# Kernel tuning notes

Hardware: AMD Instinct MI355X
Metric: run time of the kernel (lower is better)

Reference implementation:

```python
import jax, jax.numpy as jnp
import numpy as np

B, I, D = 4096, 512, 2048
MAX_DIM = 2560
LEAK_RATE = 0.2
SPIKE_THRESHOLD = 0.5


def setup_inputs() -> dict:
    key = jax.random.key(0)
    k1, k2, k3, k4, k5 = jax.random.split(key, 5)
    return {
        "inputs": jax.random.normal(k1, (B, I), dtype=jnp.float32),
        "state": jax.random.normal(k2, (B, MAX_DIM), dtype=jnp.float32),
        "W_in": jax.random.normal(k3, (D, I), dtype=jnp.float32) * 0.05,
        "W_res": jax.random.normal(k4, (D, D), dtype=jnp.float32) * 0.02,
        "W_gate": jax.random.normal(k5, (3 * D, I), dtype=jnp.float32) * 0.05,
    }


def reference(inputs, state, W_in, W_res, W_gate):
    # Slice previous state to the active reservoir dimension D.
    prev_state = state[:, :D]                                   # [B, D]
    input_part = inputs @ W_in.T                                 # [B, D]
    reservoir_part = prev_state @ W_res.T                        # [B, D]
    gate_part = jax.nn.sigmoid(inputs @ W_gate.T)                # [B, 3D]
    i_gate, f_gate, o_gate = jnp.split(gate_part, 3, axis=-1)
    new_state = (1.0 - LEAK_RATE) * (f_gate * prev_state) \
        + LEAK_RATE * jnp.tanh(i_gate * (input_part + reservoir_part))
    new_state = o_gate * new_state
    # Spike thresholding: subtract threshold where state exceeds it.
    new_state = jnp.where(new_state > SPIKE_THRESHOLD,
                          new_state - SPIKE_THRESHOLD, new_state)
    # Zero-pad active reservoir back to max_dynamic_reservoir_dim.
    padded = jnp.pad(new_state, ((0, 0), (0, MAX_DIM - D)))      # [B, MAX_DIM]
    return padded
```

## Files before the change

kernel.cpp:

```cpp
#include <hip/hip_runtime.h>
#include <math.h>


#define IDIM 512
#define DDIM 2048
#define MAXD 2560
#define BDIM 4096
#define LIST_CAP 262144
#define BAND 4e-3f

typedef __attribute__((ext_vector_type(4))) float f32x4;
typedef __attribute__((ext_vector_type(8))) _Float16 f16x8;

__device__ __forceinline__ void gld16(const unsigned short* g, unsigned short* l) {
    __builtin_amdgcn_global_load_lds((const __attribute__((address_space(1))) void*)g,
                                     (__attribute__((address_space(3))) void*)l,
                                     16, 0, 0);
}
__device__ __forceinline__ float sigf(float x) { return 1.0f / (1.0f + __expf(-x)); }

__global__ __launch_bounds__(256) void convert_kernel(
    const float* __restrict__ x, const float* __restrict__ state,
    const float* __restrict__ win, const float* __restrict__ wgate,
    const float* __restrict__ wres,
    unsigned short* __restrict__ X16, unsigned short* __restrict__ S16,
    unsigned short* __restrict__ Wc16, unsigned short* __restrict__ Wr16,
    float* __restrict__ out, unsigned* __restrict__ cnt)
{
    int idx = blockIdx.x * 256 + threadIdx.x;
    if (idx == 0) *cnt = 0u;
    float4 v;
    unsigned short* p;
    long off;
    if (idx < 524288) {
        v = ((const float4*)x)[idx];
        p = X16; off = (long)idx * 4;
    } else if (idx < 2621440) {
        int i = idx - 524288;
        int row = i >> 9, c4 = i & 511;
        v = *(const float4*)(state + (long)row * MAXD + c4 * 4);
        p = S16; off = (long)i * 4;
    } else if (idx < 3670016) {
        int i = idx - 2621440;
        v = (i < 262144) ? ((const float4*)win)[i] : ((const float4*)wgate)[i - 262144];
        p = Wc16; off = (long)i * 4;
    } else if (idx < 4718592) {
        int i = idx - 3670016;
        v = ((const float4*)wres)[i];
        p = Wr16; off = (long)i * 4;
    } else {
        int i = idx - 4718592;
        int row = i >> 7, c4 = i & 127;
        *(float4*)(out + (long)row * MAXD + DDIM + c4 * 4) = make_float4(0.f, 0.f, 0.f, 0.f);
        return;
    }
    _Float16 h0 = (_Float16)v.x, h1 = (_Float16)v.y;
    _Float16 h2 = (_Float16)v.z, h3 = (_Float16)v.w;
    ushort4 hv;
    hv.x = *(unsigned short*)&h0; hv.y = *(unsigned short*)&h1;
    hv.z = *(unsigned short*)&h2; hv.w = *(unsigned short*)&h3;
    *(ushort4*)(p + off) = hv;
}

__global__ __launch_bounds__(256, 4) void fused_step(
    const unsigned short* __restrict__ X16, const unsigned short* __restrict__ S16,
    const unsigned short* __restrict__ Wc16, const unsigned short* __restrict__ Wr16,
    const float* __restrict__ state, float* __restrict__ out,
    unsigned* __restrict__ cnt, unsigned* __restrict__ list)
{
    __shared__ alignas(16) unsigned short lA[128 * 32];
    __shared__ alignas(16) unsigned short lB[64 * 32];
    const int t = threadIdx.x;
    const int wave = t >> 6, lane = t & 63;
    const int wr = wave >> 1, wc = wave & 1;
    const int quad = lane >> 4, l16 = lane & 15;
    const int m0 = blockIdx.y * 128;
    const int n0 = blockIdx.x * 64;
    const int rowoff = lane >> 2;
    const int kg = ((lane & 3) ^ ((lane >> 3) & 3)) * 8;
    const int kr = (quad ^ ((l16 >> 1) & 3)) * 8;

    f32x4 acc[4][2];
    f32x4 u[4][2];

    #pragma unroll
    for (int mi = 0; mi < 4; mi++)
        #pragma unroll
        for (int ni = 0; ni < 2; ni++)
            acc[mi][ni] = (f32x4)0.0f;

    auto phase = [&](const unsigned short* Ag, long ldA,
                     const unsigned short* Bg, long ldB, int klen) {
        const unsigned short* a0 = Ag + (long)(wave * 32 + rowoff) * ldA + kg;
        const unsigned short* a1 = a0 + (long)16 * ldA;
        const unsigned short* b0 = Bg + (long)(wave * 16 + rowoff) * ldB + kg;
        unsigned short* dA = lA + wave * 1024;
        unsigned short* dB = lB + wave * 512;
        for (int k0 = 0; k0 < klen; k0 += 32) {
            __syncthreads();
            gld16(a0 + k0, dA);
            gld16(a1 + k0, dA + 512);
            gld16(b0 + k0, dB);
            __syncthreads();
            f16x8 af[4], bf[2];
            #pragma unroll
            for (int mi = 0; mi < 4; mi++)
                af[mi] = *(const f16x8*)&lA[(wr * 64 + mi * 16 + l16) * 32 + kr];
            #pragma unroll
            for (int ni = 0; ni < 2; ni++)
                bf[ni] = *(const f16x8*)&lB[(wc * 32 + ni * 16 + l16) * 32 + kr];
            #pragma unroll
            for (int mi = 0; mi < 4; mi++)
                #pragma unroll
                for (int ni = 0; ni < 2; ni++)
                    acc[mi][ni] = __builtin_amdgcn_mfma_f32_16x16x32_f16(af[mi], bf[ni], acc[mi][ni], 0, 0, 0);
        }
    };

    phase(S16 + (long)m0 * DDIM, DDIM, Wr16 + (long)n0 * DDIM, DDIM, DDIM);
    phase(X16 + (long)m0 * IDIM, IDIM, Wc16 + (long)n0 * IDIM, IDIM, IDIM);
    #pragma unroll
    for (int mi = 0; mi < 4; mi++)
        #pragma unroll
        for (int ni = 0; ni < 2; ni++) { u[mi][ni] = acc[mi][ni]; acc[mi][ni] = (f32x4)0.0f; }

    phase(X16 + (long)m0 * IDIM, IDIM, Wc16 + (long)(DDIM + n0) * IDIM, IDIM, IDIM);
    #pragma unroll
    for (int mi = 0; mi < 4; mi++)
        #pragma unroll
        for (int ni = 0; ni < 2; ni++) {
            #pragma unroll
            for (int r = 0; r < 4; r++)
                u[mi][ni][r] = 0.2f * tanhf(sigf(acc[mi][ni][r]) * u[mi][ni][r]);
            acc[mi][ni] = (f32x4)0.0f;
        }

    phase(X16 + (long)m0 * IDIM, IDIM, Wc16 + (long)(2 * DDIM + n0) * IDIM, IDIM, IDIM);
    #pragma unroll
    for (int mi = 0; mi < 4; mi++)
        #pragma unroll
        for (int ni = 0; ni < 2; ni++) {
            #pragma unroll
            for (int r = 0; r < 4; r++) {
                int row = m0 + wr * 64 + mi * 16 + quad * 4 + r;
                int col = n0 + wc * 32 + ni * 16 + l16;
                float prev = state[(long)row * MAXD + col];
                u[mi][ni][r] += 0.8f * sigf(acc[mi][ni][r]) * prev;
            }
            acc[mi][ni] = (f32x4)0.0f;
        }

    phase(X16 + (long)m0 * IDIM, IDIM, Wc16 + (long)(3 * DDIM + n0) * IDIM, IDIM, IDIM);
    #pragma unroll
    for (int mi = 0; mi < 4; mi++)
        #pragma unroll
        for (int ni = 0; ni < 2; ni++) {
            #pragma unroll
            for (int r = 0; r < 4; r++) {
                int row = m0 + wr * 64 + mi * 16 + quad * 4 + r;
                int col = n0 + wc * 32 + ni * 16 + l16;
                float go = sigf(acc[mi][ni][r]);
                float ns = go * u[mi][ni][r];
                float ov = (ns > 0.5f) ? ns - 0.5f : ns;
                out[(long)row * MAXD + col] = ov;
                if (fabsf(ns - 0.5f) < BAND) {
                    unsigned pos = atomicAdd(cnt, 1u);
                    if (pos < LIST_CAP) list[pos] = (unsigned)(row * DDIM + col);
                }
            }
        }
}

__global__ __launch_bounds__(256) void fixup_kernel(
    const float* __restrict__ x, const float* __restrict__ state,
    const float* __restrict__ win, const float* __restrict__ wres,
    const float* __restrict__ wgate,
    const unsigned* __restrict__ cnt, const unsigned* __restrict__ list,
    float* __restrict__ out)
{
    const int gwave = (blockIdx.x * 256 + threadIdx.x) >> 6;
    const int lane = threadIdx.x & 63;
    const int nwaves = gridDim.x * 4;
    unsigned n = *cnt;
    if (n > LIST_CAP) n = LIST_CAP;
    for (unsigned e = gwave; e < n; e += nwaves) {
        unsigned rc = list[e];
        int row = rc >> 11, col = rc & 2047;
        double ip = 0.0, gi = 0.0, gf = 0.0, go = 0.0, rp = 0.0;
        const float* xr  = x + (long)row * IDIM;
        const float* wi  = win + (long)col * IDIM;
        const float* wgi = wgate + (long)col * IDIM;
        const float* wgf = wgate + (long)(DDIM + col) * IDIM;
        const float* wgo = wgate + (long)(2 * DDIM + col) * IDIM;
        #pragma unroll
        for (int k = lane * 4; k < IDIM; k += 256) {
            float4 xv = *(const float4*)(xr + k);
            float4 a = *(const float4*)(wi + k);
            float4 b = *(const float4*)(wgi + k);
            float4 c = *(const float4*)(wgf + k);
            float4 d = *(const float4*)(wgo + k);
            ip += (double)xv.x * a.x + (double)xv.y * a.y + (double)xv.z * a.z + (double)xv.w * a.w;
            gi += (double)xv.x * b.x + (double)xv.y * b.y + (double)xv.z * b.z + (double)xv.w * b.w;
            gf += (double)xv.x * c.x + (double)xv.y * c.y + (double)xv.z * c.z + (double)xv.w * c.w;
            go += (double)xv.x * d.x + (double)xv.y * d.y + (double)xv.z * d.z + (double)xv.w * d.w;
        }
        const float* sr = state + (long)row * MAXD;
        const float* wr_ = wres + (long)col * DDIM;
        #pragma unroll 2
        for (int k = lane * 4; k < DDIM; k += 256) {
            float4 sv = *(const float4*)(sr + k);
            float4 wv = *(const float4*)(wr_ + k);
            rp += (double)sv.x * wv.x + (double)sv.y * wv.y + (double)sv.z * wv.z + (double)sv.w * wv.w;
        }
        #pragma unroll
        for (int o = 32; o > 0; o >>= 1) {
            ip += __shfl_down(ip, o);
            gi += __shfl_down(gi, o);
            gf += __shfl_down(gf, o);
            go += __shfl_down(go, o);
            rp += __shfl_down(rp, o);
        }
        if (lane == 0) {
            double si = 1.0 / (1.0 + exp(-gi));
            double sf = 1.0 / (1.0 + exp(-gf));
            double so = 1.0 / (1.0 + exp(-go));
            double prev = (double)state[(long)row * MAXD + col];
            double ns = so * (0.8 * sf * prev + 0.2 * tanh(si * (ip + rp)));
            if (ns > 0.5) ns -= 0.5;
            out[(long)row * MAXD + col] = (float)ns;
        }
    }
}

extern "C" void kernel_launch(void* const* d_in, const int* in_sizes, int n_in,
                              void* d_out, int out_size, void* d_ws, size_t ws_size,
                              hipStream_t stream) {
    const float* x     = (const float*)d_in[0];
    const float* state = (const float*)d_in[1];
    const float* win   = (const float*)d_in[2];
    const float* wres  = (const float*)d_in[3];
    const float* wgate = (const float*)d_in[4];
    float* out = (float*)d_out;

    char* ws = (char*)d_ws;
    unsigned short* X16  = (unsigned short*)(ws);
    unsigned short* S16  = (unsigned short*)(ws + (4ll  << 20));
    unsigned short* Wc16 = (unsigned short*)(ws + (20ll << 20));
    unsigned short* Wr16 = (unsigned short*)(ws + (28ll << 20));
    unsigned* cnt  = (unsigned*)(ws + (36ll << 20));
    unsigned* list = (unsigned*)(ws + (36ll << 20) + 16);

    convert_kernel<<<dim3(20480), dim3(256), 0, stream>>>(
        x, state, win, wgate, wres, X16, S16, Wc16, Wr16, out, cnt);

    fused_step<<<dim3(32, 32), dim3(256), 0, stream>>>(
        X16, S16, Wc16, Wr16, state, out, cnt, list);

    fixup_kernel<<<dim3(1024), dim3(256), 0, stream>>>(
        x, state, win, wres, wgate, cnt, list, out);
}
```

Baseline: 400.2 us.

## Enlarge GEMM tile to 128x128 with 8 waves, XCD-aware block swizzle, 16-lane fixup

```diff
diff --git a/kernel.cpp b/kernel.cpp
--- a/kernel.cpp
+++ b/kernel.cpp
@@ -62,23 +62,28 @@
     *(ushort4*)(p + off) = hv;
 }
 
-__global__ __launch_bounds__(256, 4) void fused_step(
+__global__ __launch_bounds__(512, 4) void fused_step(
     const unsigned short* __restrict__ X16, const unsigned short* __restrict__ S16,
     const unsigned short* __restrict__ Wc16, const unsigned short* __restrict__ Wr16,
     const float* __restrict__ state, float* __restrict__ out,
     unsigned* __restrict__ cnt, unsigned* __restrict__ list)
 {
     __shared__ alignas(16) unsigned short lA[128 * 32];
-    __shared__ alignas(16) unsigned short lB[64 * 32];
+    __shared__ alignas(16) unsigned short lB[128 * 32];
     const int t = threadIdx.x;
     const int wave = t >> 6, lane = t & 63;
-    const int wr = wave >> 1, wc = wave & 1;
+    const int wm = wave >> 2, wn = wave & 3;
     const int quad = lane >> 4, l16 = lane & 15;
-    const int m0 = blockIdx.y * 128;
-    const int n0 = blockIdx.x * 64;
+
+    const int bid = blockIdx.x;
+    const int nb  = (bid & 7) * 64 + (bid >> 3);
+    const int xcd = nb >> 6, lid = nb & 63;
+    const int m0 = (((xcd >> 1) << 3) + (lid >> 3)) * 128;
+    const int n0 = (((xcd & 1) << 3) + (lid & 7)) * 128;
+
     const int rowoff = lane >> 2;
     const int kg = ((lane & 3) ^ ((lane >> 3) & 3)) * 8;
-    const int kr = (quad ^ ((l16 >> 1) & 3)) * 8;
+    const int krh = (quad ^ ((l16 >> 1) & 3)) * 8;
 
     f32x4 acc[4][2];
     f32x4 u[4][2];
@@ -91,24 +96,22 @@
 
     auto phase = [&](const unsigned short* Ag, long ldA,
                      const unsigned short* Bg, long ldB, int klen) {
-        const unsigned short* a0 = Ag + (long)(wave * 32 + rowoff) * ldA + kg;
-        const unsigned short* a1 = a0 + (long)16 * ldA;
+        const unsigned short* a0 = Ag + (long)(wave * 16 + rowoff) * ldA + kg;
         const unsigned short* b0 = Bg + (long)(wave * 16 + rowoff) * ldB + kg;
-        unsigned short* dA = lA + wave * 1024;
+        unsigned short* dA = lA + wave * 512;
         unsigned short* dB = lB + wave * 512;
         for (int k0 = 0; k0 < klen; k0 += 32) {
             __syncthreads();
             gld16(a0 + k0, dA);
-            gld16(a1 + k0, dA + 512);
             gld16(b0 + k0, dB);
             __syncthreads();
             f16x8 af[4], bf[2];
             #pragma unroll
             for (int mi = 0; mi < 4; mi++)
-                af[mi] = *(const f16x8*)&lA[(wr * 64 + mi * 16 + l16) * 32 + kr];
+                af[mi] = *(const f16x8*)&lA[(wm * 64 + mi * 16 + l16) * 32 + krh];
             #pragma unroll
             for (int ni = 0; ni < 2; ni++)
-                bf[ni] = *(const f16x8*)&lB[(wc * 32 + ni * 16 + l16) * 32 + kr];
+                bf[ni] = *(const f16x8*)&lB[(wn * 32 + ni * 16 + l16) * 32 + krh];
             #pragma unroll
             for (int mi = 0; mi < 4; mi++)
                 #pragma unroll
@@ -142,8 +145,8 @@
         for (int ni = 0; ni < 2; ni++) {
             #pragma unroll
             for (int r = 0; r < 4; r++) {
-                int row = m0 + wr * 64 + mi * 16 + quad * 4 + r;
-                int col = n0 + wc * 32 + ni * 16 + l16;
+                int row = m0 + wm * 64 + mi * 16 + quad * 4 + r;
+                int col = n0 + wn * 32 + ni * 16 + l16;
                 float prev = state[(long)row * MAXD + col];
                 u[mi][ni][r] += 0.8f * sigf(acc[mi][ni][r]) * prev;
             }
@@ -157,8 +160,8 @@
         for (int ni = 0; ni < 2; ni++) {
             #pragma unroll
             for (int r = 0; r < 4; r++) {
-                int row = m0 + wr * 64 + mi * 16 + quad * 4 + r;
-                int col = n0 + wc * 32 + ni * 16 + l16;
+                int row = m0 + wm * 64 + mi * 16 + quad * 4 + r;
+                int col = n0 + wn * 32 + ni * 16 + l16;
                 float go = sigf(acc[mi][ni][r]);
                 float ns = go * u[mi][ni][r];
                 float ov = (ns > 0.5f) ? ns - 0.5f : ns;
@@ -178,12 +181,12 @@
     const unsigned* __restrict__ cnt, const unsigned* __restrict__ list,
     float* __restrict__ out)
 {
-    const int gwave = (blockIdx.x * 256 + threadIdx.x) >> 6;
-    const int lane = threadIdx.x & 63;
-    const int nwaves = gridDim.x * 4;
+    const int grp  = (blockIdx.x * 256 + threadIdx.x) >> 4;
+    const int l16  = threadIdx.x & 15;
+    const int ngrp = gridDim.x * 16;
     unsigned n = *cnt;
     if (n > LIST_CAP) n = LIST_CAP;
-    for (unsigned e = gwave; e < n; e += nwaves) {
+    for (unsigned e = grp; e < n; e += ngrp) {
         unsigned rc = list[e];
         int row = rc >> 11, col = rc & 2047;
         double ip = 0.0, gi = 0.0, gf = 0.0, go = 0.0, rp = 0.0;
@@ -192,8 +195,8 @@
         const float* wgi = wgate + (long)col * IDIM;
         const float* wgf = wgate + (long)(DDIM + col) * IDIM;
         const float* wgo = wgate + (long)(2 * DDIM + col) * IDIM;
-        #pragma unroll
-        for (int k = lane * 4; k < IDIM; k += 256) {
+        #pragma unroll 2
+        for (int k = l16 * 4; k < IDIM; k += 64) {
             float4 xv = *(const float4*)(xr + k);
             float4 a = *(const float4*)(wi + k);
             float4 b = *(const float4*)(wgi + k);
@@ -206,21 +209,21 @@
         }
         const float* sr = state + (long)row * MAXD;
         const float* wr_ = wres + (long)col * DDIM;
-        #pragma unroll 2
-        for (int k = lane * 4; k < DDIM; k += 256) {
+        #pragma unroll 4
+        for (int k = l16 * 4; k < DDIM; k += 64) {
             float4 sv = *(const float4*)(sr + k);
             float4 wv = *(const float4*)(wr_ + k);
             rp += (double)sv.x * wv.x + (double)sv.y * wv.y + (double)sv.z * wv.z + (double)sv.w * wv.w;
         }
         #pragma unroll
-        for (int o = 32; o > 0; o >>= 1) {
-            ip += __shfl_down(ip, o);
-            gi += __shfl_down(gi, o);
-            gf += __shfl_down(gf, o);
-            go += __shfl_down(go, o);
-            rp += __shfl_down(rp, o);
-        }
-        if (lane == 0) {
+        for (int o = 8; o > 0; o >>= 1) {
+            ip += __shfl_down(ip, o, 16);
+            gi += __shfl_down(gi, o, 16);
+            gf += __shfl_down(gf, o, 16);
+            go += __shfl_down(go, o, 16);
+            rp += __shfl_down(rp, o, 16);
+        }
+        if (l16 == 0) {
             double si = 1.0 / (1.0 + exp(-gi));
             double sf = 1.0 / (1.0 + exp(-gf));
             double so = 1.0 / (1.0 + exp(-go));
@@ -253,7 +256,7 @@
     convert_kernel<<<dim3(20480), dim3(256), 0, stream>>>(
         x, state, win, wgate, wres, X16, S16, Wc16, Wr16, out, cnt);
 
-    fused_step<<<dim3(32, 32), dim3(256), 0, stream>>>(
+    fused_step<<<dim3(512), dim3(512), 0, stream>>>(
         X16, S16, Wc16, Wr16, state, out, cnt, list);
 
     fixup_kernel<<<dim3(1024), dim3(256), 0, stream>>>(
```

Result: faster. 377.3 us (-5.7%).
